# Kernel optimization log

Measured on AMD Instinct MI355X. Metric: run time of the kernel, lower is better.

Reference implementation:

```python
import jax, jax.numpy as jnp
import numpy as np

TOP_K = 2


def setup_inputs() -> dict:
    key = jax.random.key(0)
    k1, k2, k3, k4, k5 = jax.random.split(key, 5)
    B, S, D, E, F = 2, 1024, 2048, 8, 768
    scale_in = 1.0 / np.sqrt(D)
    scale_ff = 1.0 / np.sqrt(F)
    return {
        "x": jax.random.normal(k1, (B, S, D), dtype=jnp.float32),
        "w_gate_router": jax.random.normal(k2, (E, D), dtype=jnp.float32) * scale_in,
        "w_gate_proj": jax.random.normal(k3, (E, F, D), dtype=jnp.float32) * scale_in,
        "w_up_proj": jax.random.normal(k4, (E, F, D), dtype=jnp.float32) * scale_in,
        "w_down_proj": jax.random.normal(k5, (E, D, F), dtype=jnp.float32) * scale_ff,
    }


def moe_forward(x, w_gate_router, w_gate_proj, w_up_proj, w_down_proj):
    E = w_gate_router.shape[0]
    # Router: scores [B,S,E], top-k selection, softmax over the k selected scores.
    scores = jnp.einsum("bsd,ed->bse", x, w_gate_router)
    topk_scores, topk_idx = jax.lax.top_k(scores, TOP_K)          # [B,S,K]
    topk_probs = jax.nn.softmax(topk_scores, axis=-1)             # [B,S,K]
    # Dense combine weights: zero for unselected experts (== scatter of topk_probs).
    weights = jnp.sum(topk_probs[..., None] * jax.nn.one_hot(topk_idx, E, dtype=x.dtype), axis=-2)  # [B,S,E]
    # Per-expert SwiGLU computed densely over all tokens (same math as
    # gather/dispatch-per-expert followed by scatter-add combine).
    gate = jnp.einsum("bsd,efd->bsef", x, w_gate_proj)            # [B,S,E,F]
    up = jnp.einsum("bsd,efd->bsef", x, w_up_proj)
    hidden = jax.nn.silu(gate) * up                                # [B,S,E,F]
    # Weighted combine: sum_e weights[b,s,e] * (hidden @ w_down[e].T)
    out = jnp.einsum("bsef,edf,bse->bsd", hidden, w_down_proj, weights)
    return out


def reference(x, w_gate_router, w_gate_proj, w_up_proj, w_down_proj):
    return moe_forward(x, w_gate_router, w_gate_proj, w_up_proj, w_down_proj)
```

## Files before the change

kernel.cpp:

```cpp
#include <hip/hip_runtime.h>

#define T_TOK 2048
#define DIM   2048
#define NEXP  8
#define FF    768
#define NGRP  16
#define BK    64

typedef unsigned short u16;
typedef unsigned int   u32;
typedef __bf16 bf16x8 __attribute__((ext_vector_type(8)));
typedef float  f32x4  __attribute__((ext_vector_type(4)));
typedef u16    u16x4  __attribute__((ext_vector_type(4)));
typedef u16    u16x8  __attribute__((ext_vector_type(8)));

#define AS1 __attribute__((address_space(1)))
#define AS3 __attribute__((address_space(3)))

__device__ __forceinline__ u16 f2bf(float f) {
    union { u32 i; float f; } v; v.f = f;
    u32 r = v.i + 0x7FFF + ((v.i >> 16) & 1);
    return (u16)(r >> 16);
}
__device__ __forceinline__ float bf2f(u16 u) {
    union { u32 i; float f; } v; v.i = ((u32)u) << 16; return v.f;
}

__device__ __forceinline__ void gload16(const u16* g, u16* l) {
    __builtin_amdgcn_global_load_lds((const AS1 u32*)g, (AS3 u32*)l, 16, 0, 0);
}

__global__ void cvtrouter_kernel(const float* __restrict__ x, const float* __restrict__ wr,
                                 int* cnt, int* rt_e, float* rt_p, u16* __restrict__ xb,
                                 const float* __restrict__ wg, u16* __restrict__ wgb,
                                 const float* __restrict__ wu, u16* __restrict__ wub,
                                 const float* __restrict__ wd, u16* __restrict__ wdb, int n4) {
    if (blockIdx.y == 0) {
        if (blockIdx.x >= T_TOK / 4) return;
        int wave = threadIdx.x >> 6, lane = threadIdx.x & 63;
        int t = blockIdx.x * 4 + wave;
        float xv[32];
#pragma unroll
        for (int i = 0; i < 32; i++) xv[i] = x[(size_t)t * DIM + i * 64 + lane];
#pragma unroll
        for (int i = 0; i < 32; i++) xb[(size_t)t * DIM + i * 64 + lane] = f2bf(xv[i]);
        float s[NEXP];
#pragma unroll
        for (int e = 0; e < NEXP; e++) {
            float acc = 0.f;
#pragma unroll
            for (int i = 0; i < 32; i++) acc += xv[i] * wr[(size_t)e * DIM + i * 64 + lane];
            for (int off = 32; off; off >>= 1) acc += __shfl_xor(acc, off);
            s[e] = acc;
        }
        if (lane == 0) {
            int bi = 0; float bv = s[0];
            for (int e = 1; e < NEXP; e++) if (s[e] > bv) { bv = s[e]; bi = e; }
            float sv = -1e30f; int si = 0;
            for (int e = 0; e < NEXP; e++) { if (e == bi) continue; if (s[e] > sv) { sv = s[e]; si = e; } }
            float p0 = 1.f / (1.f + __expf(sv - bv));
            float p1 = 1.f - p0;
            rt_e[t * 2 + 0] = bi; rt_e[t * 2 + 1] = si;
            rt_p[t * 2 + 0] = p0; rt_p[t * 2 + 1] = p1;
            atomicAdd(&cnt[bi * 2 + 0], 1);
            atomicAdd(&cnt[si * 2 + 1], 1);
        }
        return;
    }
    const float* s; u16* d;
    switch (blockIdx.y) {
        case 1: s = wg; d = wgb; break;
        case 2: s = wu; d = wub; break;
        default: s = wd; d = wdb; break;
    }
    int i = blockIdx.x * blockDim.x + threadIdx.x;
    int st = gridDim.x * blockDim.x;
    for (; i < n4; i += st) {
        f32x4 v = ((const f32x4*)s)[i];
        u16x4 o;
#pragma unroll
        for (int j = 0; j < 4; j++) o[j] = f2bf(v[j]);
        ((u16x4*)d)[i] = o;
    }
}

__global__ void scanassign_kernel(const int* cnt, const int* rt_e, const float* rt_p,
                                  int* base_g, int* tile_g, int* tile_m0, int* ntiles,
                                  int* rowtok, float* rowprob) {
    __shared__ int s_base[NGRP];
    __shared__ int s_pos[NGRP];
    int tid = threadIdx.x;
    if (tid < NGRP) s_pos[tid] = 0;
    if (tid < 64) {
        int lane = tid;
        int c = (lane < NGRP) ? cnt[lane] : 0;
        int nt_g = (c + 127) >> 7;
        int pre = 0, tpre = 0;
        for (int i = 0; i < NGRP; i++) {
            int ci = __shfl(c, i), ti = __shfl(nt_g, i);
            if (i < lane) { pre += ci; tpre += ti; }
        }
        if (lane < NGRP) {
            s_base[lane] = pre; base_g[lane] = pre;
            for (int j = 0; j < nt_g; j++) { tile_g[tpre + j] = lane; tile_m0[tpre + j] = j * 128; }
            if (lane == NGRP - 1) *ntiles = tpre + nt_g;
        }
    }
    __syncthreads();
    for (int t = tid; t < T_TOK; t += 256) {
#pragma unroll
        for (int k = 0; k < 2; k++) {
            int g = rt_e[t * 2 + k] * 2 + k;
            int pos = atomicAdd(&s_pos[g], 1);
            int row = s_base[g] + pos;
            rowtok[row] = t;
            rowprob[row] = rt_p[t * 2 + k];
        }
    }
}

__launch_bounds__(256)
__global__ void gateup_kernel(const u16* __restrict__ xb, const u16* __restrict__ wgb,
                              const u16* __restrict__ wub,
                              const int* cnt, const int* base, const int* tile_g,
                              const int* tile_m0, const int* ntiles,
                              const int* rowtok, const float* rowprob,
                              u16* __restrict__ hidden) {
    int tile = blockIdx.x;
    if (tile >= *ntiles) return;
    int g = tile_g[tile], m0 = tile_m0[tile];
    int e = g >> 1;
    int f0 = blockIdx.y * 64;
    int cg = cnt[g], bg_ = base[g];

    __shared__ u16 As[2][128 * BK];
    __shared__ u16 Bs[2][128 * BK];
    __shared__ int   tks[128];
    __shared__ float ps[128];

    int tid = threadIdx.x;
    if (tid < 128) {
        int valid = (m0 + tid) < cg;
        tks[tid] = valid ? rowtok[bg_ + m0 + tid] : 0;
        ps[tid]  = valid ? rowprob[bg_ + m0 + tid] : 0.f;
    }
    __syncthreads();

    int wave = tid >> 6, lane = tid & 63;
    int quad = lane >> 4, l16 = lane & 15;
    int wr = wave >> 1, wc = wave & 1;

    int r8  = lane >> 3;
    int csw = ((lane & 7) ^ r8) * 8;

    const u16* gA[4]; int lA[4];
#pragma unroll
    for (int gi = 0; gi < 4; gi++) {
        int row = wave * 32 + gi * 8 + r8;
        gA[gi] = xb + (size_t)tks[row] * DIM + csw;
        lA[gi] = (wave * 32 + gi * 8) * BK;
    }
    const u16* bsrc = (wave >> 1) ? wub : wgb;
    int fo = (wave & 1) * 8 + r8;
    const u16* gB[4]; int lB[4];
#pragma unroll
    for (int gi = 0; gi < 4; gi++) {
        gB[gi] = bsrc + ((size_t)e * FF + f0 + gi * 16 + fo) * DIM + csw;
        lB[gi] = (gi * 32 + wave * 8) * BK;
    }

    f32x4 acc[4][4] = {};

#pragma unroll
    for (int gi = 0; gi < 4; gi++) gload16(gA[gi], &As[0][0] + lA[gi]);
#pragma unroll
    for (int gi = 0; gi < 4; gi++) gload16(gB[gi], &Bs[0][0] + lB[gi]);
    __syncthreads();

    int sw0 = ((0 * 4 + quad) ^ (l16 & 7)) * 8;
    int sw1 = ((1 * 4 + quad) ^ (l16 & 7)) * 8;

#pragma unroll 2
    for (int kt = 0; kt < DIM / BK; kt++) {
        int cur = kt & 1;
        int kk = (kt + 1) * BK;
        if (kk < DIM) {
#pragma unroll
            for (int gi = 0; gi < 4; gi++) gload16(gA[gi] + kk, &As[cur ^ 1][0] + lA[gi]);
#pragma unroll
            for (int gi = 0; gi < 4; gi++) gload16(gB[gi] + kk, &Bs[cur ^ 1][0] + lB[gi]);
        }
#pragma unroll
        for (int ks = 0; ks < 2; ks++) {
            int sw = ks ? sw1 : sw0;
            bf16x8 a[4], b[4];
#pragma unroll
            for (int mi = 0; mi < 4; mi++)
                a[mi] = *(const bf16x8*)&As[cur][(wr * 64 + mi * 16 + l16) * BK + sw];
#pragma unroll
            for (int ni = 0; ni < 4; ni++)
                b[ni] = *(const bf16x8*)&Bs[cur][(wc * 64 + ni * 16 + l16) * BK + sw];
#pragma unroll
            for (int mi = 0; mi < 4; mi++)
#pragma unroll
                for (int ni = 0; ni < 4; ni++)
                    acc[mi][ni] = __builtin_amdgcn_mfma_f32_16x16x32_bf16(a[mi], b[ni], acc[mi][ni], 0, 0, 0);
        }
        __syncthreads();
    }

    int fb = f0 + wc * 32 + l16;
#pragma unroll
    for (int mi = 0; mi < 4; mi++) {
#pragma unroll
        for (int r = 0; r < 4; r++) {
            int m = wr * 64 + mi * 16 + quad * 4 + r;
            if (m0 + m < cg) {
                float p = ps[m];
                float g0 = acc[mi][0][r], u0 = acc[mi][1][r];
                float g1 = acc[mi][2][r], u1 = acc[mi][3][r];
                size_t rowo = (size_t)(bg_ + m0 + m) * FF;
                hidden[rowo + fb]      = f2bf((g0 / (1.f + __expf(-g0))) * u0 * p);
                hidden[rowo + fb + 16] = f2bf((g1 / (1.f + __expf(-g1))) * u1 * p);
            }
        }
    }
}

__launch_bounds__(256)
__global__ void down_kernel(const u16* __restrict__ hid, const u16* __restrict__ wdb,
                            const int* cnt, const int* base, const int* tile_g,
                            const int* tile_m0, const int* ntiles, const int* rowtok,
                            u16* __restrict__ out0, u16* __restrict__ out1) {
    int tile = blockIdx.x;
    if (tile >= *ntiles) return;
    int g = tile_g[tile], m0 = tile_m0[tile];
    int e = g >> 1, slot = g & 1;
    int d0 = blockIdx.y * 128;
    int cg = cnt[g], bg_ = base[g];

    __shared__ u16 As[2][128 * BK];
    __shared__ u16 Bs[2][128 * BK];
    __shared__ int tks[128];

    int tid = threadIdx.x;
    if (tid < 128) tks[tid] = ((m0 + tid) < cg) ? rowtok[bg_ + m0 + tid] : 0;
    __syncthreads();

    int wave = tid >> 6, lane = tid & 63;
    int quad = lane >> 4, l16 = lane & 15;
    int wr = wave >> 1, wc = wave & 1;

    int r8  = lane >> 3;
    int csw = ((lane & 7) ^ r8) * 8;

    const u16* gA[4]; int lA[4];
#pragma unroll
    for (int gi = 0; gi < 4; gi++) {
        int row = wave * 32 + gi * 8 + r8;
        gA[gi] = hid + (size_t)(bg_ + m0 + row) * FF + csw;
        lA[gi] = (wave * 32 + gi * 8) * BK;
    }
    const u16* gB[4]; int lB[4];
#pragma unroll
    for (int gi = 0; gi < 4; gi++) {
        int n = gi * 32 + wave * 8 + r8;
        gB[gi] = wdb + ((size_t)e * DIM + d0 + n) * FF + csw;
        lB[gi] = (gi * 32 + wave * 8) * BK;
    }

    f32x4 acc[4][4] = {};

#pragma unroll
    for (int gi = 0; gi < 4; gi++) gload16(gA[gi], &As[0][0] + lA[gi]);
#pragma unroll
    for (int gi = 0; gi < 4; gi++) gload16(gB[gi], &Bs[0][0] + lB[gi]);
    __syncthreads();

    int sw0 = ((0 * 4 + quad) ^ (l16 & 7)) * 8;
    int sw1 = ((1 * 4 + quad) ^ (l16 & 7)) * 8;

#pragma unroll 2
    for (int kt = 0; kt < FF / BK; kt++) {
        int cur = kt & 1;
        int kk = (kt + 1) * BK;
        if (kk < FF) {
#pragma unroll
            for (int gi = 0; gi < 4; gi++) gload16(gA[gi] + kk, &As[cur ^ 1][0] + lA[gi]);
#pragma unroll
            for (int gi = 0; gi < 4; gi++) gload16(gB[gi] + kk, &Bs[cur ^ 1][0] + lB[gi]);
        }
#pragma unroll
        for (int ks = 0; ks < 2; ks++) {
            int sw = ks ? sw1 : sw0;
            bf16x8 a[4], b[4];
#pragma unroll
            for (int mi = 0; mi < 4; mi++)
                a[mi] = *(const bf16x8*)&As[cur][(wr * 64 + mi * 16 + l16) * BK + sw];
#pragma unroll
            for (int ni = 0; ni < 4; ni++)
                b[ni] = *(const bf16x8*)&Bs[cur][(wc * 64 + ni * 16 + l16) * BK + sw];
#pragma unroll
            for (int mi = 0; mi < 4; mi++)
#pragma unroll
                for (int ni = 0; ni < 4; ni++)
                    acc[mi][ni] = __builtin_amdgcn_mfma_f32_16x16x32_bf16(a[mi], b[ni], acc[mi][ni], 0, 0, 0);
        }
        __syncthreads();
    }

    u16* outp = slot ? out1 : out0;
#pragma unroll
    for (int mi = 0; mi < 4; mi++) {
#pragma unroll
        for (int ni = 0; ni < 4; ni++) {
            int d = d0 + wc * 64 + ni * 16 + l16;
#pragma unroll
            for (int r = 0; r < 4; r++) {
                int m = wr * 64 + mi * 16 + quad * 4 + r;
                if (m0 + m < cg) {
                    outp[(size_t)tks[m] * DIM + d] = f2bf(acc[mi][ni][r]);
                }
            }
        }
    }
}

__global__ void combine_kernel(const u16* __restrict__ o0, const u16* __restrict__ o1,
                               float* __restrict__ out) {
    int i = blockIdx.x * blockDim.x + threadIdx.x;
    u16x8 a = *(const u16x8*)(o0 + (size_t)i * 8);
    u16x8 b = *(const u16x8*)(o1 + (size_t)i * 8);
    f32x4 r0, r1;
#pragma unroll
    for (int j = 0; j < 4; j++) {
        r0[j] = bf2f(a[j]) + bf2f(b[j]);
        r1[j] = bf2f(a[4 + j]) + bf2f(b[4 + j]);
    }
    *(f32x4*)(out + (size_t)i * 8) = r0;
    *(f32x4*)(out + (size_t)i * 8 + 4) = r1;
}

extern "C" void kernel_launch(void* const* d_in, const int* in_sizes, int n_in,
                              void* d_out, int out_size, void* d_ws, size_t ws_size,
                              hipStream_t stream) {
    const float* x  = (const float*)d_in[0];
    const float* wr = (const float*)d_in[1];
    const float* wg = (const float*)d_in[2];
    const float* wu = (const float*)d_in[3];
    const float* wd = (const float*)d_in[4];
    float* out = (float*)d_out;

    char* W = (char*)d_ws;
    int*   cnt     = (int*)(W + 0);
    int*   base    = (int*)(W + 128);
    int*   ntiles  = (int*)(W + 192);
    int*   tile_g  = (int*)(W + 256);
    int*   tile_m0 = (int*)(W + 512);
    int*   rt_e    = (int*)(W + 1024);
    float* rt_p    = (float*)(W + 20480);
    int*   rowtok  = (int*)(W + 40960);
    float* rowprob = (float*)(W + 61440);
    u16*   hidden  = (u16*)(W + 81920);
    u16*   xb      = (u16*)(W + ((size_t)8  << 20));
    u16*   wgb     = (u16*)(W + ((size_t)17 << 20));
    u16*   wub     = (u16*)(W + ((size_t)43 << 20));
    u16*   wdb     = (u16*)(W + ((size_t)69 << 20));
    u16*   out0    = (u16*)(W + ((size_t)17 << 20));
    u16*   out1    = (u16*)(W + ((size_t)26 << 20));

    hipMemsetAsync(W, 0, 256, stream);

    const int NW = NEXP * FF * DIM / 4;
    cvtrouter_kernel<<<dim3(1536, 4), 256, 0, stream>>>(x, wr, cnt, rt_e, rt_p, xb,
                                                        wg, wgb, wu, wub, wd, wdb, NW);
    scanassign_kernel<<<1, 256, 0, stream>>>(cnt, rt_e, rt_p, base, tile_g, tile_m0,
                                             ntiles, rowtok, rowprob);

    gateup_kernel<<<dim3(48, 12), 256, 0, stream>>>(xb, wgb, wub, cnt, base, tile_g, tile_m0,
                                                    ntiles, rowtok, rowprob, hidden);
    down_kernel<<<dim3(48, 16), 256, 0, stream>>>(hidden, wdb, cnt, base, tile_g, tile_m0,
                                                  ntiles, rowtok, out0, out1);
    combine_kernel<<<T_TOK * DIM / (256 * 8), 256, 0, stream>>>(out0, out1, out);
}
```

Before: 362.5 us.

## Fuse fp32-to-bf16 weight conversion into GEMM B-tile loads

Drops the separate pass that converted all expert weights to bf16 in the workspace. The gate/up and down GEMMs now read fp32 weights directly into registers, convert them to bf16, and write them to swizzled LDS for the next k-step. This avoids a full read and write of the weight tensors, but each weight tile is re-read and re-converted by every token tile that uses that expert. B loads also move from async global-to-LDS loads to register-staged loads, which raises register pressure and weakens overlap with compute.

Measured after the change: 397.0 us. +9.5%, slower.

```diff
diff --git a/kernel.cpp b/kernel.cpp
--- a/kernel.cpp
+++ b/kernel.cpp
@@ -30,57 +30,35 @@
     __builtin_amdgcn_global_load_lds((const AS1 u32*)g, (AS3 u32*)l, 16, 0, 0);
 }
 
-__global__ void cvtrouter_kernel(const float* __restrict__ x, const float* __restrict__ wr,
-                                 int* cnt, int* rt_e, float* rt_p, u16* __restrict__ xb,
-                                 const float* __restrict__ wg, u16* __restrict__ wgb,
-                                 const float* __restrict__ wu, u16* __restrict__ wub,
-                                 const float* __restrict__ wd, u16* __restrict__ wdb, int n4) {
-    if (blockIdx.y == 0) {
-        if (blockIdx.x >= T_TOK / 4) return;
-        int wave = threadIdx.x >> 6, lane = threadIdx.x & 63;
-        int t = blockIdx.x * 4 + wave;
-        float xv[32];
-#pragma unroll
-        for (int i = 0; i < 32; i++) xv[i] = x[(size_t)t * DIM + i * 64 + lane];
-#pragma unroll
-        for (int i = 0; i < 32; i++) xb[(size_t)t * DIM + i * 64 + lane] = f2bf(xv[i]);
-        float s[NEXP];
-#pragma unroll
-        for (int e = 0; e < NEXP; e++) {
-            float acc = 0.f;
-#pragma unroll
-            for (int i = 0; i < 32; i++) acc += xv[i] * wr[(size_t)e * DIM + i * 64 + lane];
-            for (int off = 32; off; off >>= 1) acc += __shfl_xor(acc, off);
-            s[e] = acc;
-        }
-        if (lane == 0) {
-            int bi = 0; float bv = s[0];
-            for (int e = 1; e < NEXP; e++) if (s[e] > bv) { bv = s[e]; bi = e; }
-            float sv = -1e30f; int si = 0;
-            for (int e = 0; e < NEXP; e++) { if (e == bi) continue; if (s[e] > sv) { sv = s[e]; si = e; } }
-            float p0 = 1.f / (1.f + __expf(sv - bv));
-            float p1 = 1.f - p0;
-            rt_e[t * 2 + 0] = bi; rt_e[t * 2 + 1] = si;
-            rt_p[t * 2 + 0] = p0; rt_p[t * 2 + 1] = p1;
-            atomicAdd(&cnt[bi * 2 + 0], 1);
-            atomicAdd(&cnt[si * 2 + 1], 1);
-        }
-        return;
-    }
-    const float* s; u16* d;
-    switch (blockIdx.y) {
-        case 1: s = wg; d = wgb; break;
-        case 2: s = wu; d = wub; break;
-        default: s = wd; d = wdb; break;
-    }
-    int i = blockIdx.x * blockDim.x + threadIdx.x;
-    int st = gridDim.x * blockDim.x;
-    for (; i < n4; i += st) {
-        f32x4 v = ((const f32x4*)s)[i];
-        u16x4 o;
-#pragma unroll
-        for (int j = 0; j < 4; j++) o[j] = f2bf(v[j]);
-        ((u16x4*)d)[i] = o;
+__global__ void router_kernel(const float* __restrict__ x, const float* __restrict__ wr,
+                              int* cnt, int* rt_e, float* rt_p, u16* __restrict__ xb) {
+    int wave = threadIdx.x >> 6, lane = threadIdx.x & 63;
+    int t = blockIdx.x * 4 + wave;
+    float xv[32];
+#pragma unroll
+    for (int i = 0; i < 32; i++) xv[i] = x[(size_t)t * DIM + i * 64 + lane];
+#pragma unroll
+    for (int i = 0; i < 32; i++) xb[(size_t)t * DIM + i * 64 + lane] = f2bf(xv[i]);
+    float s[NEXP];
+#pragma unroll
+    for (int e = 0; e < NEXP; e++) {
+        float acc = 0.f;
+#pragma unroll
+        for (int i = 0; i < 32; i++) acc += xv[i] * wr[(size_t)e * DIM + i * 64 + lane];
+        for (int off = 32; off; off >>= 1) acc += __shfl_xor(acc, off);
+        s[e] = acc;
+    }
+    if (lane == 0) {
+        int bi = 0; float bv = s[0];
+        for (int e = 1; e < NEXP; e++) if (s[e] > bv) { bv = s[e]; bi = e; }
+        float sv = -1e30f; int si = 0;
+        for (int e = 0; e < NEXP; e++) { if (e == bi) continue; if (s[e] > sv) { sv = s[e]; si = e; } }
+        float p0 = 1.f / (1.f + __expf(sv - bv));
+        float p1 = 1.f - p0;
+        rt_e[t * 2 + 0] = bi; rt_e[t * 2 + 1] = si;
+        rt_p[t * 2 + 0] = p0; rt_p[t * 2 + 1] = p1;
+        atomicAdd(&cnt[bi * 2 + 0], 1);
+        atomicAdd(&cnt[si * 2 + 1], 1);
     }
 }
 
@@ -120,8 +98,8 @@
 }
 
 __launch_bounds__(256)
-__global__ void gateup_kernel(const u16* __restrict__ xb, const u16* __restrict__ wgb,
-                              const u16* __restrict__ wub,
+__global__ void gateup_kernel(const u16* __restrict__ xb, const float* __restrict__ wg,
+                              const float* __restrict__ wu,
                               const int* cnt, const int* base, const int* tile_g,
                               const int* tile_m0, const int* ntiles,
                               const int* rowtok, const float* rowprob,
@@ -151,7 +129,10 @@
     int wr = wave >> 1, wc = wave & 1;
 
     int r8  = lane >> 3;
-    int csw = ((lane & 7) ^ r8) * 8;
+    int c   = lane & 7;
+    int csw = (c ^ r8) * 8;
+    int c8  = c * 8;
+    int bsw = (c ^ r8) * 8;
 
     const u16* gA[4]; int lA[4];
 #pragma unroll
@@ -160,21 +141,29 @@
         gA[gi] = xb + (size_t)tks[row] * DIM + csw;
         lA[gi] = (wave * 32 + gi * 8) * BK;
     }
-    const u16* bsrc = (wave >> 1) ? wub : wgb;
+    const float* bsrcf = (wave >> 1) ? wu : wg;
     int fo = (wave & 1) * 8 + r8;
-    const u16* gB[4]; int lB[4];
-#pragma unroll
-    for (int gi = 0; gi < 4; gi++) {
-        gB[gi] = bsrc + ((size_t)e * FF + f0 + gi * 16 + fo) * DIM + csw;
-        lB[gi] = (gi * 32 + wave * 8) * BK;
+    const float* gBf[4]; int lB[4];
+#pragma unroll
+    for (int gi = 0; gi < 4; gi++) {
+        gBf[gi] = bsrcf + ((size_t)e * FF + f0 + gi * 16 + fo) * DIM + c8;
+        lB[gi] = (gi * 32 + wave * 8 + r8) * BK + bsw;
     }
 
     f32x4 acc[4][4] = {};
+    f32x4 b0[4], b1[4];
 
 #pragma unroll
     for (int gi = 0; gi < 4; gi++) gload16(gA[gi], &As[0][0] + lA[gi]);
 #pragma unroll
-    for (int gi = 0; gi < 4; gi++) gload16(gB[gi], &Bs[0][0] + lB[gi]);
+    for (int gi = 0; gi < 4; gi++) { b0[gi] = *(const f32x4*)(gBf[gi]); b1[gi] = *(const f32x4*)(gBf[gi] + 4); }
+#pragma unroll
+    for (int gi = 0; gi < 4; gi++) {
+        u16x8 o;
+#pragma unroll
+        for (int j = 0; j < 4; j++) { o[j] = f2bf(b0[gi][j]); o[4 + j] = f2bf(b1[gi][j]); }
+        *(u16x8*)&Bs[0][lB[gi]] = o;
+    }
     __syncthreads();
 
     int sw0 = ((0 * 4 + quad) ^ (l16 & 7)) * 8;
@@ -188,7 +177,7 @@
 #pragma unroll
             for (int gi = 0; gi < 4; gi++) gload16(gA[gi] + kk, &As[cur ^ 1][0] + lA[gi]);
 #pragma unroll
-            for (int gi = 0; gi < 4; gi++) gload16(gB[gi] + kk, &Bs[cur ^ 1][0] + lB[gi]);
+            for (int gi = 0; gi < 4; gi++) { b0[gi] = *(const f32x4*)(gBf[gi] + kk); b1[gi] = *(const f32x4*)(gBf[gi] + kk + 4); }
         }
 #pragma unroll
         for (int ks = 0; ks < 2; ks++) {
@@ -205,6 +194,15 @@
 #pragma unroll
                 for (int ni = 0; ni < 4; ni++)
                     acc[mi][ni] = __builtin_amdgcn_mfma_f32_16x16x32_bf16(a[mi], b[ni], acc[mi][ni], 0, 0, 0);
+        }
+        if (kk < DIM) {
+#pragma unroll
+            for (int gi = 0; gi < 4; gi++) {
+                u16x8 o;
+#pragma unroll
+                for (int j = 0; j < 4; j++) { o[j] = f2bf(b0[gi][j]); o[4 + j] = f2bf(b1[gi][j]); }
+                *(u16x8*)&Bs[cur ^ 1][lB[gi]] = o;
+            }
         }
         __syncthreads();
     }
@@ -228,7 +226,7 @@
 }
 
 __launch_bounds__(256)
-__global__ void down_kernel(const u16* __restrict__ hid, const u16* __restrict__ wdb,
+__global__ void down_kernel(const u16* __restrict__ hid, const float* __restrict__ wd,
                             const int* cnt, const int* base, const int* tile_g,
                             const int* tile_m0, const int* ntiles, const int* rowtok,
                             u16* __restrict__ out0, u16* __restrict__ out1) {
@@ -252,7 +250,10 @@
     int wr = wave >> 1, wc = wave & 1;
 
     int r8  = lane >> 3;
-    int csw = ((lane & 7) ^ r8) * 8;
+    int c   = lane & 7;
+    int csw = (c ^ r8) * 8;
+    int c8  = c * 8;
+    int bsw = (c ^ r8) * 8;
 
     const u16* gA[4]; int lA[4];
 #pragma unroll
@@ -261,20 +262,28 @@
         gA[gi] = hid + (size_t)(bg_ + m0 + row) * FF + csw;
         lA[gi] = (wave * 32 + gi * 8) * BK;
     }
-    const u16* gB[4]; int lB[4];
+    const float* gBf[4]; int lB[4];
 #pragma unroll
     for (int gi = 0; gi < 4; gi++) {
         int n = gi * 32 + wave * 8 + r8;
-        gB[gi] = wdb + ((size_t)e * DIM + d0 + n) * FF + csw;
-        lB[gi] = (gi * 32 + wave * 8) * BK;
+        gBf[gi] = wd + ((size_t)e * DIM + d0 + n) * FF + c8;
+        lB[gi] = n * BK + bsw;
     }
 
     f32x4 acc[4][4] = {};
+    f32x4 b0[4], b1[4];
 
 #pragma unroll
     for (int gi = 0; gi < 4; gi++) gload16(gA[gi], &As[0][0] + lA[gi]);
 #pragma unroll
-    for (int gi = 0; gi < 4; gi++) gload16(gB[gi], &Bs[0][0] + lB[gi]);
+    for (int gi = 0; gi < 4; gi++) { b0[gi] = *(const f32x4*)(gBf[gi]); b1[gi] = *(const f32x4*)(gBf[gi] + 4); }
+#pragma unroll
+    for (int gi = 0; gi < 4; gi++) {
+        u16x8 o;
+#pragma unroll
+        for (int j = 0; j < 4; j++) { o[j] = f2bf(b0[gi][j]); o[4 + j] = f2bf(b1[gi][j]); }
+        *(u16x8*)&Bs[0][lB[gi]] = o;
+    }
     __syncthreads();
 
     int sw0 = ((0 * 4 + quad) ^ (l16 & 7)) * 8;
@@ -288,7 +297,7 @@
 #pragma unroll
             for (int gi = 0; gi < 4; gi++) gload16(gA[gi] + kk, &As[cur ^ 1][0] + lA[gi]);
 #pragma unroll
-            for (int gi = 0; gi < 4; gi++) gload16(gB[gi] + kk, &Bs[cur ^ 1][0] + lB[gi]);
+            for (int gi = 0; gi < 4; gi++) { b0[gi] = *(const f32x4*)(gBf[gi] + kk); b1[gi] = *(const f32x4*)(gBf[gi] + kk + 4); }
         }
 #pragma unroll
         for (int ks = 0; ks < 2; ks++) {
@@ -305,6 +314,15 @@
 #pragma unroll
                 for (int ni = 0; ni < 4; ni++)
                     acc[mi][ni] = __builtin_amdgcn_mfma_f32_16x16x32_bf16(a[mi], b[ni], acc[mi][ni], 0, 0, 0);
+        }
+        if (kk < FF) {
+#pragma unroll
+            for (int gi = 0; gi < 4; gi++) {
+                u16x8 o;
+#pragma unroll
+                for (int j = 0; j < 4; j++) { o[j] = f2bf(b0[gi][j]); o[4 + j] = f2bf(b1[gi][j]); }
+                *(u16x8*)&Bs[cur ^ 1][lB[gi]] = o;
+            }
         }
         __syncthreads();
     }
@@ -363,23 +381,18 @@
     float* rowprob = (float*)(W + 61440);
     u16*   hidden  = (u16*)(W + 81920);
     u16*   xb      = (u16*)(W + ((size_t)8  << 20));
-    u16*   wgb     = (u16*)(W + ((size_t)17 << 20));
-    u16*   wub     = (u16*)(W + ((size_t)43 << 20));
-    u16*   wdb     = (u16*)(W + ((size_t)69 << 20));
     u16*   out0    = (u16*)(W + ((size_t)17 << 20));
     u16*   out1    = (u16*)(W + ((size_t)26 << 20));
 
     hipMemsetAsync(W, 0, 256, stream);
 
-    const int NW = NEXP * FF * DIM / 4;
-    cvtrouter_kernel<<<dim3(1536, 4), 256, 0, stream>>>(x, wr, cnt, rt_e, rt_p, xb,
-                                                        wg, wgb, wu, wub, wd, wdb, NW);
+    router_kernel<<<T_TOK / 4, 256, 0, stream>>>(x, wr, cnt, rt_e, rt_p, xb);
     scanassign_kernel<<<1, 256, 0, stream>>>(cnt, rt_e, rt_p, base, tile_g, tile_m0,
                                              ntiles, rowtok, rowprob);
 
-    gateup_kernel<<<dim3(48, 12), 256, 0, stream>>>(xb, wgb, wub, cnt, base, tile_g, tile_m0,
+    gateup_kernel<<<dim3(48, 12), 256, 0, stream>>>(xb, wg, wu, cnt, base, tile_g, tile_m0,
                                                     ntiles, rowtok, rowprob, hidden);
-    down_kernel<<<dim3(48, 16), 256, 0, stream>>>(hidden, wdb, cnt, base, tile_g, tile_m0,
+    down_kernel<<<dim3(48, 16), 256, 0, stream>>>(hidden, wd, cnt, base, tile_g, tile_m0,
                                                   ntiles, rowtok, out0, out1);
     combine_kernel<<<T_TOK * DIM / (256 * 8), 256, 0, stream>>>(out0, out1, out);
 }
```
